# Kernel tuning notes

Measured on AMD Instinct MI355X. Metric: run time of the kernel, lower is better.

Reference implementation:

```python
import jax, jax.numpy as jnp
import numpy as np
from jax import lax

B, N, D = 8, 1024, 2
MAX_ITERS = 100
REG = 0.1
INNER = 10  # convergence check cadence (cpt % 10 == 0 in the torch code)
TOL = 1e-3


def setup_inputs() -> dict:
    key = jax.random.key(0)
    k1, k2, k3, k4 = jax.random.split(key, 4)
    return {
        "coord1": jax.random.normal(k1, (B, N, D), jnp.float32),
        "prob1": jax.random.uniform(k2, (B, N), jnp.float32),
        "coord2": jax.random.normal(k3, (B, N, D), jnp.float32),
        "prob2": jax.random.uniform(k4, (B, N), jnp.float32),
    }


def _pairwise_sq(x, y):
    # squared euclidean distance, [B, N, N]; same math as the torch cat/broadcast version
    return jnp.sum((x[:, :, None, :] - y[:, None, :, :]) ** 2, axis=-1)


def _sinkhorn(a, b, M):
    bsz, n = a.shape
    a = a[..., None]                      # [B, n, 1]
    b = b[..., None]                      # [B, n, 1]
    K = jnp.exp(-M / REG)                 # [B, n, n]
    Kt = jnp.swapaxes(K, 1, 2)
    u0 = jnp.full((bsz, n, 1), 1.0 / n, M.dtype)
    v0 = jnp.full((bsz, n, 1), 1.0 / n, M.dtype)
    P0 = u0 * K * jnp.swapaxes(v0, 1, 2)
    done0 = jnp.array(False)

    def inner(c, _):
        u, v, done = c
        KtU = jnp.matmul(Kt, u)           # [B, n, 1]
        v1 = b / KtU
        u1 = a / jnp.matmul(K, v1)
        bad = jnp.any(KtU == 0) | ~(jnp.all(jnp.isfinite(u1)) & jnp.all(jnp.isfinite(v1)))
        ok = ~(done | bad)                # freeze updates after break (numerical error)
        return (jnp.where(ok, u1, u), jnp.where(ok, v1, v), done | bad), None

    def outer(c, _):
        u, v, P, done = c
        (u, v, done2), _ = lax.scan(inner, (u, v, done), None, length=INNER)
        Pn = u * K * jnp.swapaxes(v, 1, 2)
        upd = ~done2                      # skip P update if bad/converged already
        conv = jnp.max(jnp.abs(P - Pn)) < TOL
        P = jnp.where(upd, Pn, P)
        return (u, v, P, done2 | (upd & conv)), None

    (_, _, P, _), _ = lax.scan(outer, (u0, v0, P0, done0), None, length=MAX_ITERS // INNER)
    return P


def reference(coord1, prob1, coord2, prob2):
    M = _pairwise_sq(coord1, coord2)
    M = M / jnp.max(M, axis=(1, 2), keepdims=True)
    a = prob1 + 1e-8
    a = a / jnp.sum(a, axis=1, keepdims=True)
    bb = prob2 + 1e-8
    bb = bb / jnp.sum(bb, axis=1, keepdims=True)
    return _sinkhorn(a, bb, M)
```

## Files before the change

### kernel.cpp

```cpp
#include <hip/hip_runtime.h>
#include <hip/hip_fp16.h>

#define NPTS 1024
#define BATCH 8
#define BPB 32
#define NBLOCKS (BATCH * BPB)
#define NTHREADS 512
#define WPB 8
#define RPW 4
#define KCH 16
#define KP  8

#define SCOPE_AGENT __HIP_MEMORY_SCOPE_AGENT

typedef unsigned long long ull;

constexpr float REG_ = 0.1f;
constexpr float LOG2E = 1.4426950408889634f;
constexpr unsigned POISON = 0xAAAAAAAAu;

__device__ __forceinline__ float wave_sum(float x) {
    #pragma unroll
    for (int off = 32; off; off >>= 1) x += __shfl_xor(x, off);
    return x;
}
__device__ __forceinline__ float wave_max(float x) {
    #pragma unroll
    for (int off = 32; off; off >>= 1) x = fmaxf(x, __shfl_xor(x, off));
    return x;
}

__global__ __launch_bounds__(NTHREADS, 2) void sinkhorn_fused(
    const float2* __restrict__ c1g, const float* __restrict__ p1g,
    const float2* __restrict__ c2g, const float* __restrict__ p2g,
    float* __restrict__ out, unsigned* __restrict__ cnt_all,
    int* __restrict__ mmw_all, ull* __restrict__ upk_all,
    ull* __restrict__ vpk_all)
{
    const int tid  = threadIdx.x;
    const int lane = tid & 63;
    const int w    = tid >> 6;
    const int bid  = blockIdx.x & (BATCH - 1);
    const int sub  = blockIdx.x >> 3;
    const int gb   = bid << 10;
    const int r0   = sub * 32 + w * RPW;

    unsigned* cnt = cnt_all + bid * 32;
    int*      mmw = mmw_all + bid * 32;
    ull* upk = upk_all + (gb >> 1);
    ull* vpk = vpk_all + (gb >> 1);

    __shared__ float xe[NPTS];
    __shared__ float red[WPB];
    __shared__ float smax;

    float s1 = 0.f, s2 = 0.f;
    #pragma unroll
    for (int k = 0; k < KCH; ++k) {
        int t = lane + 64 * k;
        s1 += p1g[gb + t] + 1e-8f;
        s2 += p2g[gb + t] + 1e-8f;
    }
    s1 = wave_sum(s1);
    s2 = wave_sum(s2);

    float rc1x[RPW], rc1y[RPW], rc2x[RPW], rc2y[RPW], pa[RPW], pb[RPW];
    #pragma unroll
    for (int i = 0; i < RPW; ++i) {
        float2 c1 = c1g[gb + r0 + i];
        float2 c2 = c2g[gb + r0 + i];
        rc1x[i] = c1.x; rc1y[i] = c1.y;
        rc2x[i] = c2.x; rc2y[i] = c2.y;
        pa[i] = (p1g[gb + r0 + i] + 1e-8f) / s1;
        pb[i] = (p2g[gb + r0 + i] + 1e-8f) / s2;
    }

    float m = 0.f;
    #pragma unroll
    for (int k = 0; k < KCH; ++k) {
        float2 c = c2g[gb + lane + 64 * k];
        #pragma unroll
        for (int i = 0; i < RPW; ++i) {
            float dx = rc1x[i] - c.x, dy = rc1y[i] - c.y;
            m = fmaxf(m, dx * dx + dy * dy);
        }
    }
    m = wave_max(m);
    if (lane == 0) red[w] = m;
    __syncthreads();

    unsigned tgt = POISON + BPB;
    if (tid == 0) {
        float bm = red[0];
        #pragma unroll
        for (int i = 1; i < WPB; ++i) bm = fmaxf(bm, red[i]);
        __hip_atomic_fetch_max(mmw, (int)__float_as_uint(bm),
                               __ATOMIC_RELAXED, SCOPE_AGENT);
        asm volatile("s_waitcnt vmcnt(0)" ::: "memory");
        __hip_atomic_fetch_add(cnt, 1u, __ATOMIC_RELAXED, SCOPE_AGENT);
        while ((int)(__hip_atomic_load(cnt, __ATOMIC_RELAXED, SCOPE_AGENT) - tgt) < 0) {}
        smax = __uint_as_float((unsigned)
            __hip_atomic_load(mmw, __ATOMIC_RELAXED, SCOPE_AGENT));
    }
    __syncthreads();
    const float mmax = smax;
    const float nIL2 = -LOG2E / (REG_ * mmax);

    __half2 Kupk[RPW][KP], Kvpk[RPW][KP];
    #pragma unroll
    for (int p = 0; p < KP; ++p) {
        float2 cA = c2g[gb + lane + 128 * p];
        float2 cB = c2g[gb + lane + 128 * p + 64];
        #pragma unroll
        for (int i = 0; i < RPW; ++i) {
            float dxa = rc1x[i] - cA.x, dya = rc1y[i] - cA.y;
            float dxb = rc1x[i] - cB.x, dyb = rc1y[i] - cB.y;
            Kupk[i][p] = __floats2half2_rn(exp2f(nIL2 * (dxa * dxa + dya * dya)),
                                           exp2f(nIL2 * (dxb * dxb + dyb * dyb)));
        }
        float2 cC = c1g[gb + lane + 128 * p];
        float2 cD = c1g[gb + lane + 128 * p + 64];
        #pragma unroll
        for (int i = 0; i < RPW; ++i) {
            float dxa = rc2x[i] - cC.x, dya = rc2y[i] - cC.y;
            float dxb = rc2x[i] - cD.x, dyb = rc2y[i] - cD.y;
            Kvpk[i][p] = __floats2half2_rn(exp2f(nIL2 * (dxa * dxa + dya * dya)),
                                           exp2f(nIL2 * (dxb * dxb + dyb * dyb)));
        }
    }

    const int sa = (w << 6) + lane;
    float accu[RPW];
    float vcp[KCH];
    for (int it = 0; it < 10; ++it) {
        float acc[RPW] = {0.f, 0.f, 0.f, 0.f};
        if (it == 0) {
            #pragma unroll
            for (int p = 0; p < KP; ++p)
                #pragma unroll
                for (int i = 0; i < RPW; ++i) {
                    float2 kf = __half22float2(Kvpk[i][p]);
                    acc[i] += kf.x + kf.y;
                }
            #pragma unroll
            for (int i = 0; i < RPW; ++i) acc[i] *= (1.0f / NPTS);
        } else {
            #pragma unroll
            for (int p = 0; p < KP; ++p) {
                float x0 = xe[128 * p + lane];
                float x1 = xe[128 * p + 64 + lane];
                #pragma unroll
                for (int i = 0; i < RPW; ++i) {
                    float2 kf = __half22float2(Kvpk[i][p]);
                    acc[i] = fmaf(kf.x, x0, fmaf(kf.y, x1, acc[i]));
                }
            }
        }
        #pragma unroll
        for (int i = 0; i < RPW; ++i) acc[i] = wave_sum(acc[i]);
        if (lane == 0) {
            float v0 = pb[0] / acc[0], v1 = pb[1] / acc[1];
            float v2 = pb[2] / acc[2], v3 = pb[3] / acc[3];
            __hip_atomic_store(&vpk[r0 >> 1],
                ((ull)__float_as_uint(v1) << 32) | __float_as_uint(v0),
                __ATOMIC_RELAXED, SCOPE_AGENT);
            __hip_atomic_store(&vpk[(r0 >> 1) + 1],
                ((ull)__float_as_uint(v3) << 32) | __float_as_uint(v2),
                __ATOMIC_RELAXED, SCOPE_AGENT);
        }
        __syncthreads();
        tgt += BPB;
        if (tid == 0) {
            __hip_atomic_fetch_add(cnt, 1u, __ATOMIC_RELAXED, SCOPE_AGENT);
            while ((int)(__hip_atomic_load(cnt, __ATOMIC_RELAXED, SCOPE_AGENT) - tgt) < 0) {}
        }
        __syncthreads();
        {
            ull r = __hip_atomic_load(&vpk[sa], __ATOMIC_RELAXED, SCOPE_AGENT);
            ((float2*)xe)[sa] = make_float2(__uint_as_float((unsigned)r),
                                            __uint_as_float((unsigned)(r >> 32)));
        }
        __syncthreads();

        #pragma unroll
        for (int i = 0; i < RPW; ++i) accu[i] = 0.f;
        #pragma unroll
        for (int p = 0; p < KP; ++p) {
            float x0 = xe[128 * p + lane];
            float x1 = xe[128 * p + 64 + lane];
            if (it == 9) { vcp[2 * p] = x0; vcp[2 * p + 1] = x1; }
            #pragma unroll
            for (int i = 0; i < RPW; ++i) {
                float2 kf = __half22float2(Kupk[i][p]);
                accu[i] = fmaf(kf.x, x0, fmaf(kf.y, x1, accu[i]));
            }
        }
        #pragma unroll
        for (int i = 0; i < RPW; ++i) accu[i] = wave_sum(accu[i]);
        if (it < 9) {
            if (lane == 0) {
                float u0 = pa[0] / accu[0], u1 = pa[1] / accu[1];
                float u2 = pa[2] / accu[2], u3 = pa[3] / accu[3];
                __hip_atomic_store(&upk[r0 >> 1],
                    ((ull)__float_as_uint(u1) << 32) | __float_as_uint(u0),
                    __ATOMIC_RELAXED, SCOPE_AGENT);
                __hip_atomic_store(&upk[(r0 >> 1) + 1],
                    ((ull)__float_as_uint(u3) << 32) | __float_as_uint(u2),
                    __ATOMIC_RELAXED, SCOPE_AGENT);
            }
            __syncthreads();
            tgt += BPB;
            if (tid == 0) {
                __hip_atomic_fetch_add(cnt, 1u, __ATOMIC_RELAXED, SCOPE_AGENT);
                while ((int)(__hip_atomic_load(cnt, __ATOMIC_RELAXED, SCOPE_AGENT) - tgt) < 0) {}
            }
            __syncthreads();
            ull r = __hip_atomic_load(&upk[sa], __ATOMIC_RELAXED, SCOPE_AGENT);
            ((float2*)xe)[sa] = make_float2(__uint_as_float((unsigned)r),
                                            __uint_as_float((unsigned)(r >> 32)));
            __syncthreads();
        }
    }

    float rowu[RPW];
    #pragma unroll
    for (int i = 0; i < RPW; ++i) rowu[i] = pa[i] / accu[i];
    const long ob = ((long)bid << 20) + ((long)r0 << 10);
    #pragma unroll
    for (int p = 0; p < KP; ++p) {
        #pragma unroll
        for (int i = 0; i < RPW; ++i) {
            float2 kf = __half22float2(Kupk[i][p]);
            __builtin_nontemporal_store(rowu[i] * kf.x * vcp[2 * p],
                &out[ob + (i << 10) + 128 * p + lane]);
            __builtin_nontemporal_store(rowu[i] * kf.y * vcp[2 * p + 1],
                &out[ob + (i << 10) + 128 * p + 64 + lane]);
        }
    }
}

extern "C" void kernel_launch(void* const* d_in, const int* in_sizes, int n_in,
                              void* d_out, int out_size, void* d_ws, size_t ws_size,
                              hipStream_t stream) {
    const float2* c1 = (const float2*)d_in[0];
    const float*  p1 = (const float*)d_in[1];
    const float2* c2 = (const float2*)d_in[2];
    const float*  p2 = (const float*)d_in[3];
    float* out = (float*)d_out;

    unsigned* cnt = (unsigned*)d_ws;
    int*      mmw = (int*)((char*)d_ws + 1024);
    ull* upk = (ull*)((char*)d_ws + 2048);
    ull* vpk = upk + BATCH * NPTS / 2;

    sinkhorn_fused<<<NBLOCKS, NTHREADS, 0, stream>>>(c1, p1, c2, p2, out,
                                                     cnt, mmw, upk, vpk);
}
```

Before: 120.3 us.

## Use 1024-thread blocks with half the blocks per batch and vectorized float4 accesses

Halves the number of blocks per batch from 32 to 16 by doubling threads per block to 1024, so each inter-block barrier waits on fewer arrivals. Column accesses change from strided float2 loads to float4 loads, covering global coordinate and probability reads, shared-memory reads of u/v, and the final output stores. Each lane now owns four contiguous columns instead of two interleaved pairs. The grid becomes 128 blocks of 16 waves, which puts fewer CUs to work per batch and may lower occupancy per CU.

```diff
diff --git a/kernel.cpp b/kernel.cpp
--- a/kernel.cpp
+++ b/kernel.cpp
@@ -3,17 +3,17 @@
 
 #define NPTS 1024
 #define BATCH 8
-#define BPB 32
+#define BPB 16
 #define NBLOCKS (BATCH * BPB)
-#define NTHREADS 512
-#define WPB 8
+#define NTHREADS 1024
+#define WPB 16
 #define RPW 4
-#define KCH 16
-#define KP  8
+#define KQ  4
 
 #define SCOPE_AGENT __HIP_MEMORY_SCOPE_AGENT
 
 typedef unsigned long long ull;
+typedef float f4 __attribute__((ext_vector_type(4)));
 
 constexpr float REG_ = 0.1f;
 constexpr float LOG2E = 1.4426950408889634f;
@@ -30,7 +30,7 @@
     return x;
 }
 
-__global__ __launch_bounds__(NTHREADS, 2) void sinkhorn_fused(
+__global__ __launch_bounds__(NTHREADS, 4) void sinkhorn_fused(
     const float2* __restrict__ c1g, const float* __restrict__ p1g,
     const float2* __restrict__ c2g, const float* __restrict__ p2g,
     float* __restrict__ out, unsigned* __restrict__ cnt_all,
@@ -43,28 +43,36 @@
     const int bid  = blockIdx.x & (BATCH - 1);
     const int sub  = blockIdx.x >> 3;
     const int gb   = bid << 10;
-    const int r0   = sub * 32 + w * RPW;
+    const int r0   = sub * 64 + w * RPW;
 
     unsigned* cnt = cnt_all + bid * 32;
     int*      mmw = mmw_all + bid * 32;
     ull* upk = upk_all + (gb >> 1);
     ull* vpk = vpk_all + (gb >> 1);
 
-    __shared__ float xe[NPTS];
-    __shared__ float red[WPB];
-    __shared__ float smax;
+    __shared__ float4 xe4[NPTS / 4];
+    __shared__ float  red[WPB];
+    __shared__ float  smax;
+    float2* xe2 = (float2*)xe4;
+
+    const float4* p1g4 = (const float4*)(p1g + gb);
+    const float4* p2g4 = (const float4*)(p2g + gb);
+    const float4* c1g4 = (const float4*)(c1g + gb);
+    const float4* c2g4 = (const float4*)(c2g + gb);
 
     float s1 = 0.f, s2 = 0.f;
     #pragma unroll
-    for (int k = 0; k < KCH; ++k) {
-        int t = lane + 64 * k;
-        s1 += p1g[gb + t] + 1e-8f;
-        s2 += p2g[gb + t] + 1e-8f;
+    for (int q = 0; q < KQ; ++q) {
+        float4 a = p1g4[64 * q + lane];
+        float4 b = p2g4[64 * q + lane];
+        s1 += (a.x + a.y) + (a.z + a.w) + 4e-8f;
+        s2 += (b.x + b.y) + (b.z + b.w) + 4e-8f;
     }
     s1 = wave_sum(s1);
     s2 = wave_sum(s2);
 
-    float rc1x[RPW], rc1y[RPW], rc2x[RPW], rc2y[RPW], pa[RPW], pb[RPW];
+    float rc1x[RPW], rc1y[RPW], pa[RPW], pb[RPW];
+    float rc2x[RPW], rc2y[RPW];
     #pragma unroll
     for (int i = 0; i < RPW; ++i) {
         float2 c1 = c1g[gb + r0 + i];
@@ -77,12 +85,17 @@
 
     float m = 0.f;
     #pragma unroll
-    for (int k = 0; k < KCH; ++k) {
-        float2 c = c2g[gb + lane + 64 * k];
-        #pragma unroll
-        for (int i = 0; i < RPW; ++i) {
-            float dx = rc1x[i] - c.x, dy = rc1y[i] - c.y;
-            m = fmaxf(m, dx * dx + dy * dy);
+    for (int q = 0; q < KQ; ++q) {
+        float4 A = c2g4[128 * q + 2 * lane];
+        float4 B = c2g4[128 * q + 2 * lane + 1];
+        #pragma unroll
+        for (int i = 0; i < RPW; ++i) {
+            float dx0 = rc1x[i] - A.x, dy0 = rc1y[i] - A.y;
+            float dx1 = rc1x[i] - A.z, dy1 = rc1y[i] - A.w;
+            float dx2 = rc1x[i] - B.x, dy2 = rc1y[i] - B.y;
+            float dx3 = rc1x[i] - B.z, dy3 = rc1y[i] - B.w;
+            m = fmaxf(m, fmaxf(fmaxf(dx0 * dx0 + dy0 * dy0, dx1 * dx1 + dy1 * dy1),
+                               fmaxf(dx2 * dx2 + dy2 * dy2, dx3 * dx3 + dy3 * dy3)));
         }
     }
     m = wave_max(m);
@@ -106,53 +119,62 @@
     const float mmax = smax;
     const float nIL2 = -LOG2E / (REG_ * mmax);
 
-    __half2 Kupk[RPW][KP], Kvpk[RPW][KP];
-    #pragma unroll
-    for (int p = 0; p < KP; ++p) {
-        float2 cA = c2g[gb + lane + 128 * p];
-        float2 cB = c2g[gb + lane + 128 * p + 64];
-        #pragma unroll
-        for (int i = 0; i < RPW; ++i) {
-            float dxa = rc1x[i] - cA.x, dya = rc1y[i] - cA.y;
-            float dxb = rc1x[i] - cB.x, dyb = rc1y[i] - cB.y;
-            Kupk[i][p] = __floats2half2_rn(exp2f(nIL2 * (dxa * dxa + dya * dya)),
-                                           exp2f(nIL2 * (dxb * dxb + dyb * dyb)));
-        }
-        float2 cC = c1g[gb + lane + 128 * p];
-        float2 cD = c1g[gb + lane + 128 * p + 64];
-        #pragma unroll
-        for (int i = 0; i < RPW; ++i) {
-            float dxa = rc2x[i] - cC.x, dya = rc2y[i] - cC.y;
-            float dxb = rc2x[i] - cD.x, dyb = rc2y[i] - cD.y;
-            Kvpk[i][p] = __floats2half2_rn(exp2f(nIL2 * (dxa * dxa + dya * dya)),
-                                           exp2f(nIL2 * (dxb * dxb + dyb * dyb)));
-        }
-    }
-
-    const int sa = (w << 6) + lane;
+    __half2 Kupk[RPW][KQ][2], Kvpk[RPW][KQ][2];
+    #pragma unroll
+    for (int q = 0; q < KQ; ++q) {
+        float4 A = c2g4[128 * q + 2 * lane];
+        float4 B = c2g4[128 * q + 2 * lane + 1];
+        #pragma unroll
+        for (int i = 0; i < RPW; ++i) {
+            float dx0 = rc1x[i] - A.x, dy0 = rc1y[i] - A.y;
+            float dx1 = rc1x[i] - A.z, dy1 = rc1y[i] - A.w;
+            float dx2 = rc1x[i] - B.x, dy2 = rc1y[i] - B.y;
+            float dx3 = rc1x[i] - B.z, dy3 = rc1y[i] - B.w;
+            Kupk[i][q][0] = __floats2half2_rn(exp2f(nIL2 * (dx0 * dx0 + dy0 * dy0)),
+                                              exp2f(nIL2 * (dx1 * dx1 + dy1 * dy1)));
+            Kupk[i][q][1] = __floats2half2_rn(exp2f(nIL2 * (dx2 * dx2 + dy2 * dy2)),
+                                              exp2f(nIL2 * (dx3 * dx3 + dy3 * dy3)));
+        }
+        float4 C = c1g4[128 * q + 2 * lane];
+        float4 D = c1g4[128 * q + 2 * lane + 1];
+        #pragma unroll
+        for (int i = 0; i < RPW; ++i) {
+            float dx0 = rc2x[i] - C.x, dy0 = rc2y[i] - C.y;
+            float dx1 = rc2x[i] - C.z, dy1 = rc2y[i] - C.w;
+            float dx2 = rc2x[i] - D.x, dy2 = rc2y[i] - D.y;
+            float dx3 = rc2x[i] - D.z, dy3 = rc2y[i] - D.w;
+            Kvpk[i][q][0] = __floats2half2_rn(exp2f(nIL2 * (dx0 * dx0 + dy0 * dy0)),
+                                              exp2f(nIL2 * (dx1 * dx1 + dy1 * dy1)));
+            Kvpk[i][q][1] = __floats2half2_rn(exp2f(nIL2 * (dx2 * dx2 + dy2 * dy2)),
+                                              exp2f(nIL2 * (dx3 * dx3 + dy3 * dy3)));
+        }
+    }
+
     float accu[RPW];
-    float vcp[KCH];
+    float4 vcq[KQ];
     for (int it = 0; it < 10; ++it) {
         float acc[RPW] = {0.f, 0.f, 0.f, 0.f};
         if (it == 0) {
             #pragma unroll
-            for (int p = 0; p < KP; ++p)
+            for (int q = 0; q < KQ; ++q)
                 #pragma unroll
                 for (int i = 0; i < RPW; ++i) {
-                    float2 kf = __half22float2(Kvpk[i][p]);
-                    acc[i] += kf.x + kf.y;
+                    float2 k0 = __half22float2(Kvpk[i][q][0]);
+                    float2 k1 = __half22float2(Kvpk[i][q][1]);
+                    acc[i] += (k0.x + k0.y) + (k1.x + k1.y);
                 }
             #pragma unroll
             for (int i = 0; i < RPW; ++i) acc[i] *= (1.0f / NPTS);
         } else {
             #pragma unroll
-            for (int p = 0; p < KP; ++p) {
-                float x0 = xe[128 * p + lane];
-                float x1 = xe[128 * p + 64 + lane];
+            for (int q = 0; q < KQ; ++q) {
+                float4 x = xe4[64 * q + lane];
                 #pragma unroll
                 for (int i = 0; i < RPW; ++i) {
-                    float2 kf = __half22float2(Kvpk[i][p]);
-                    acc[i] = fmaf(kf.x, x0, fmaf(kf.y, x1, acc[i]));
+                    float2 k0 = __half22float2(Kvpk[i][q][0]);
+                    float2 k1 = __half22float2(Kvpk[i][q][1]);
+                    acc[i] = fmaf(k0.x, x.x, fmaf(k0.y, x.y,
+                             fmaf(k1.x, x.z, fmaf(k1.y, x.w, acc[i]))));
                 }
             }
         }
@@ -161,10 +183,11 @@
         if (lane == 0) {
             float v0 = pb[0] / acc[0], v1 = pb[1] / acc[1];
             float v2 = pb[2] / acc[2], v3 = pb[3] / acc[3];
-            __hip_atomic_store(&vpk[r0 >> 1],
+            const int at = sub * 32 + w * 2;
+            __hip_atomic_store(&vpk[at],
                 ((ull)__float_as_uint(v1) << 32) | __float_as_uint(v0),
                 __ATOMIC_RELAXED, SCOPE_AGENT);
-            __hip_atomic_store(&vpk[(r0 >> 1) + 1],
+            __hip_atomic_store(&vpk[at + 1],
                 ((ull)__float_as_uint(v3) << 32) | __float_as_uint(v2),
                 __ATOMIC_RELAXED, SCOPE_AGENT);
         }
@@ -175,24 +198,25 @@
             while ((int)(__hip_atomic_load(cnt, __ATOMIC_RELAXED, SCOPE_AGENT) - tgt) < 0) {}
         }
         __syncthreads();
-        {
-            ull r = __hip_atomic_load(&vpk[sa], __ATOMIC_RELAXED, SCOPE_AGENT);
-            ((float2*)xe)[sa] = make_float2(__uint_as_float((unsigned)r),
-                                            __uint_as_float((unsigned)(r >> 32)));
+        if (tid < 512) {
+            ull r = __hip_atomic_load(&vpk[tid], __ATOMIC_RELAXED, SCOPE_AGENT);
+            xe2[tid] = make_float2(__uint_as_float((unsigned)r),
+                                   __uint_as_float((unsigned)(r >> 32)));
         }
         __syncthreads();
 
         #pragma unroll
         for (int i = 0; i < RPW; ++i) accu[i] = 0.f;
         #pragma unroll
-        for (int p = 0; p < KP; ++p) {
-            float x0 = xe[128 * p + lane];
-            float x1 = xe[128 * p + 64 + lane];
-            if (it == 9) { vcp[2 * p] = x0; vcp[2 * p + 1] = x1; }
+        for (int q = 0; q < KQ; ++q) {
+            float4 x = xe4[64 * q + lane];
+            if (it == 9) vcq[q] = x;
             #pragma unroll
             for (int i = 0; i < RPW; ++i) {
-                float2 kf = __half22float2(Kupk[i][p]);
-                accu[i] = fmaf(kf.x, x0, fmaf(kf.y, x1, accu[i]));
+                float2 k0 = __half22float2(Kupk[i][q][0]);
+                float2 k1 = __half22float2(Kupk[i][q][1]);
+                accu[i] = fmaf(k0.x, x.x, fmaf(k0.y, x.y,
+                          fmaf(k1.x, x.z, fmaf(k1.y, x.w, accu[i]))));
             }
         }
         #pragma unroll
@@ -201,10 +225,11 @@
             if (lane == 0) {
                 float u0 = pa[0] / accu[0], u1 = pa[1] / accu[1];
                 float u2 = pa[2] / accu[2], u3 = pa[3] / accu[3];
-                __hip_atomic_store(&upk[r0 >> 1],
+                const int at = sub * 32 + w * 2;
+                __hip_atomic_store(&upk[at],
                     ((ull)__float_as_uint(u1) << 32) | __float_as_uint(u0),
                     __ATOMIC_RELAXED, SCOPE_AGENT);
-                __hip_atomic_store(&upk[(r0 >> 1) + 1],
+                __hip_atomic_store(&upk[at + 1],
                     ((ull)__float_as_uint(u3) << 32) | __float_as_uint(u2),
                     __ATOMIC_RELAXED, SCOPE_AGENT);
             }
@@ -215,9 +240,11 @@
                 while ((int)(__hip_atomic_load(cnt, __ATOMIC_RELAXED, SCOPE_AGENT) - tgt) < 0) {}
             }
             __syncthreads();
-            ull r = __hip_atomic_load(&upk[sa], __ATOMIC_RELAXED, SCOPE_AGENT);
-            ((float2*)xe)[sa] = make_float2(__uint_as_float((unsigned)r),
-                                            __uint_as_float((unsigned)(r >> 32)));
+            if (tid < 512) {
+                ull r = __hip_atomic_load(&upk[tid], __ATOMIC_RELAXED, SCOPE_AGENT);
+                xe2[tid] = make_float2(__uint_as_float((unsigned)r),
+                                       __uint_as_float((unsigned)(r >> 32)));
+            }
             __syncthreads();
         }
     }
@@ -225,16 +252,20 @@
     float rowu[RPW];
     #pragma unroll
     for (int i = 0; i < RPW; ++i) rowu[i] = pa[i] / accu[i];
-    const long ob = ((long)bid << 20) + ((long)r0 << 10);
-    #pragma unroll
-    for (int p = 0; p < KP; ++p) {
-        #pragma unroll
-        for (int i = 0; i < RPW; ++i) {
-            float2 kf = __half22float2(Kupk[i][p]);
-            __builtin_nontemporal_store(rowu[i] * kf.x * vcp[2 * p],
-                &out[ob + (i << 10) + 128 * p + lane]);
-            __builtin_nontemporal_store(rowu[i] * kf.y * vcp[2 * p + 1],
-                &out[ob + (i << 10) + 128 * p + 64 + lane]);
+    f4* out4 = (f4*)out;
+    const long ob4 = ((long)bid << 18) + ((long)r0 << 8);
+    #pragma unroll
+    for (int q = 0; q < KQ; ++q) {
+        #pragma unroll
+        for (int i = 0; i < RPW; ++i) {
+            float2 k0 = __half22float2(Kupk[i][q][0]);
+            float2 k1 = __half22float2(Kupk[i][q][1]);
+            f4 r;
+            r.x = rowu[i] * k0.x * vcq[q].x;
+            r.y = rowu[i] * k0.y * vcq[q].y;
+            r.z = rowu[i] * k1.x * vcq[q].z;
+            r.w = rowu[i] * k1.y * vcq[q].w;
+            __builtin_nontemporal_store(r, &out4[ob4 + (i << 8) + 64 * q + lane]);
         }
     }
 }
```

Result: slower. 294.9 us (+145.1%).
